# Performance work log

Measured on AMD Instinct MI355X. Metric: run time of the kernel, lower is better.

Reference implementation:

```python
import jax, jax.numpy as jnp
import numpy as np

EPS = 1e-5
INF = 1e5


def setup_inputs() -> dict:
    key = jax.random.key(0)
    ks = iter(jax.random.split(key, 32))
    B, N, F, H, NH, C = 2, 384, 64, 64, 4, 32
    def lin(k, fi, fo):
        return jax.random.normal(k, (fi, fo), jnp.float32) / np.sqrt(fi).astype(np.float32)
    d = {}
    d['h'] = jax.random.normal(next(ks), (B, N, F), jnp.float32)
    d['x'] = jax.random.normal(next(ks), (B, N, 3), jnp.float32)
    # edge_model (ConcatenationFilter): Linear(2F+1,H), SiLU, Linear(H,H), SiLU
    d['We0'] = lin(next(ks), 2 * F + 1, H); d['be0'] = jnp.zeros(H, jnp.float32)
    d['We1'] = lin(next(ks), H, H);         d['be1'] = jnp.zeros(H, jnp.float32)
    # semantic_attention_mlp: Linear(H, n_heads), LeakyReLU(0.2)
    d['Ws'] = lin(next(ks), H, NH);         d['bs'] = jnp.zeros(NH, jnp.float32)
    # coefficients_mlp: Linear(H,H), SiLU, Linear(H,C)
    d['Wc0'] = lin(next(ks), H, H);         d['bc0'] = jnp.zeros(H, jnp.float32)
    d['Wc1'] = lin(next(ks), H, C);         d['bc1'] = jnp.zeros(C, jnp.float32)
    # post_norm_mlp: Linear(C,H), SiLU, Linear(H,H)
    d['Wp0'] = lin(next(ks), C, H);         d['bp0'] = jnp.zeros(H, jnp.float32)
    d['Wp1'] = lin(next(ks), H, H);         d['bp1'] = jnp.zeros(H, jnp.float32)
    # coordinate_mlp: Linear(H,H), SiLU, Linear(H,1,bias=False) init gain 1e-3
    d['Wx0'] = lin(next(ks), H, H);         d['bx0'] = jnp.zeros(H, jnp.float32)
    d['Wx1'] = lin(next(ks), H, 1) * 1e-3
    # node_mlp: Linear(NH*H + H + F, H), SiLU, Linear(H, F)
    d['Wn0'] = lin(next(ks), NH * H + H + F, H); d['bn0'] = jnp.zeros(H, jnp.float32)
    d['Wn1'] = lin(next(ks), H, F);         d['bn1'] = jnp.zeros(F, jnp.float32)
    d['log_gamma'] = jnp.zeros(NH, jnp.float32)
    return d


def _forward(h, x, We0, be0, We1, be1, Ws, bs, Wc0, bc0, Wc1, bc1,
             Wp0, bp0, Wp1, bp1, Wx0, bx0, Wx1, Wn0, bn0, Wn1, bn1, log_gamma):
    B, N, F = h.shape
    silu = jax.nn.silu

    # pairwise displacements and distances: (B,N,N,3), (B,N,N,1)
    x_minus_xt = x[:, :, None, :] - x[:, None, :, :]
    norm = jnp.sqrt(jnp.sum(x_minus_xt * x_minus_xt, axis=-1, keepdims=True) + EPS)

    # pairwise node-feature concat + distance -> edge MLP (ConcatenationFilter)
    hi = jnp.broadcast_to(h[:, :, None, :], (B, N, N, F))
    hj = jnp.broadcast_to(h[:, None, :, :], (B, N, N, F))
    e_in = jnp.concatenate([hi, hj, norm], axis=-1)           # (B,N,N,2F+1)
    h_e = silu(silu(e_in @ We0 + be0) @ We1 + be1)            # (B,N,N,H)

    eye = jnp.eye(N, dtype=h.dtype)[None, :, :, None]         # mask self-edges

    # euclidean attention per head, softmax over neighbors j (axis=-2)
    eu = jax.nn.softmax(-(norm + INF * eye) * jnp.exp(log_gamma), axis=-2)  # (B,N,N,NH)
    # semantic attention
    sem_logits = jax.nn.leaky_relu(h_e @ Ws + bs, 0.2) - INF * eye
    sem = jax.nn.softmax(sem_logits, axis=-2)                 # (B,N,N,NH)
    comb = eu * sem
    comb = comb / (jnp.sum(comb, axis=-2, keepdims=True) + EPS)

    # attention-weighted multi-head edge features, aggregated over neighbors
    h_e_att = (comb[..., :, None] * h_e[..., None, :]).reshape(B, N, N, -1)  # (B,N,N,NH*H)
    h_e_agg = jnp.sum(h_e_att, axis=-2)                       # (B,N,NH*H)

    # spatial attention: equivariant combinations of unit direction vectors
    coeff = silu(h_e @ Wc0 + bc0) @ Wc1 + bc1                 # (B,N,N,C)
    x_hat = x_minus_xt / (norm + EPS)                         # (B,N,N,3)
    combinations = coeff[..., :, None] * x_hat[..., None, :]  # (B,N,N,C,3)
    comb_sum = jnp.mean(combinations, axis=2)                 # mean over j -> (B,N,C,3)
    comb_norm = jnp.sum(comb_sum * comb_sum, axis=-1)         # (B,N,C)
    h_comb = silu(comb_norm @ Wp0 + bp0) @ Wp1 + bp1          # (B,N,H)

    # node update (residual)
    node_in = jnp.concatenate([h, h_e_agg, h_comb], axis=-1)
    h_out = h + (silu(node_in @ Wn0 + bn0) @ Wn1 + bn1)

    # coordinate update: scalar-gated displacements, mean over neighbors
    scale = silu(h_e @ Wx0 + bx0) @ Wx1                       # (B,N,N,1)
    x_out = x + jnp.mean(x_minus_xt * scale, axis=2)          # (B,N,3)
    return h_out, x_out


def reference(h, x, We0, be0, We1, be1, Ws, bs, Wc0, bc0, Wc1, bc1,
              Wp0, bp0, Wp1, bp1, Wx0, bx0, Wx1, Wn0, bn0, Wn1, bn1, log_gamma):
    return _forward(h, x, We0, be0, We1, be1, Ws, bs, Wc0, bc0, Wc1, bc1,
                    Wp0, bp0, Wp1, bp1, Wx0, bx0, Wx1, Wn0, bn0, Wn1, bn1, log_gamma)
```

## Files before the change

### kernel.cpp

```cpp
#include <hip/hip_runtime.h>

#define NPT 384
#define NB 2
#define NROW (NB*NPT)
#define NT 6
#define HOFF 49152
#define RECB 1024
#define REC_OFF 424960

typedef unsigned short u16;
typedef unsigned int u32;
typedef __bf16 bf16x8 __attribute__((ext_vector_type(8)));
typedef float f32x4 __attribute__((ext_vector_type(4)));

struct alignas(16) U4 { u32 x, y, z, w; };

constexpr float kEPS = 1e-5f;
constexpr float kINF = 1e5f;

__device__ __forceinline__ u16 f2b(float f) { __bf16 b = (__bf16)f; return __builtin_bit_cast(u16, b); }
__device__ __forceinline__ u32 pk2(float lo, float hi) { return (u32)f2b(lo) | ((u32)f2b(hi) << 16); }
__device__ __forceinline__ float b2f(u32 u) { return __uint_as_float(u << 16); }
__device__ __forceinline__ float silu_f(float v) { return v * __builtin_amdgcn_rcpf(1.f + __expf(-v)); }
__device__ __forceinline__ float wredmax(float v) {
#pragma unroll
  for (int m = 32; m >= 1; m >>= 1) v = fmaxf(v, __shfl_xor(v, m, 64));
  return v;
}
__device__ __forceinline__ float wredsum(float v) {
#pragma unroll
  for (int m = 32; m >= 1; m >>= 1) v += __shfl_xor(v, m, 64);
  return v;
}
__device__ __forceinline__ void up8(U4 u, float* f) {
  f[0] = b2f(u.x & 0xffffu); f[1] = b2f(u.x >> 16);
  f[2] = b2f(u.y & 0xffffu); f[3] = b2f(u.y >> 16);
  f[4] = b2f(u.z & 0xffffu); f[5] = b2f(u.z >> 16);
  f[6] = b2f(u.w & 0xffffu); f[7] = b2f(u.w >> 16);
}

__global__ __launch_bounds__(64) void sake_prep(
    const float* __restrict__ h, const float* __restrict__ We0,
    const float* __restrict__ be0, const float* __restrict__ We1,
    const float* __restrict__ Wc0, const float* __restrict__ Wc1,
    const float* __restrict__ Wx0, const float* __restrict__ Ws,
    float* __restrict__ U, float* __restrict__ V, u16* __restrict__ WT)
{
  const int t = threadIdx.x;
  const int blk = blockIdx.x;
  if (blk < NROW) {
    __shared__ float hs[64];
    hs[t] = h[blk * 64 + t];
    __syncthreads();
    float u = be0[t], v = 0.f;
#pragma unroll 8
    for (int k = 0; k < 64; k++) {
      float hv = hs[k];
      u = fmaf(hv, We0[k * 64 + t], u);
      v = fmaf(hv, We0[(64 + k) * 64 + t], v);
    }
    U[blk * 64 + t] = u;
    V[blk * 64 + t] = v;
  } else {
    const int wsel = blk - NROW;
    if (wsel == 4) {
      u16* dst = WT + 14336;
      for (int o = t; o < 16 * 64; o += 64) {
        int c = o >> 6, k = o & 63;
        dst[o] = (c < 4) ? f2b(Ws[k * 4 + c]) : (u16)0;
      }
      return;
    }
    const float* src; int nout; u16* dst;
    if      (wsel == 0) { src = We1; nout = 64; dst = WT;         }
    else if (wsel == 1) { src = Wc0; nout = 64; dst = WT + 4096;  }
    else if (wsel == 2) { src = Wx0; nout = 64; dst = WT + 8192;  }
    else                { src = Wc1; nout = 32; dst = WT + 12288; }
    const int total = 64 * nout;
    for (int o = t; o < total; o += 64) {
      int n = o >> 6, k = o & 63;
      dst[o] = f2b(src[k * nout + n]);
    }
  }
}

struct MainArgs {
  const float *x, *U, *V;
  const u16 *We1T, *Wc0T, *Wx0T, *Wc1T, *WsPT;
  const float *We0, *bs, *be1, *bc0, *bc1, *bx0, *Wx1, *log_gamma;
  char* rec;
};

__device__ __forceinline__ void readB(const u16* tile, int j, int kg, bf16x8& f0, bf16x8& f1) {
  const int r7 = j & 7;
  f0 = *(const bf16x8*)(tile + j * 64 + ((kg ^ r7) << 3));
  f1 = *(const bf16x8*)(tile + j * 64 + (((kg + 4) ^ r7) << 3));
}

template<int NNT, bool SILU_, int NCH, bool DUALT>
__device__ __forceinline__ void gemmT8(const u16* __restrict__ wG, const float* __restrict__ biasG,
                                       bf16x8 bf0, bf16x8 bf1, u16* out, u16* oTT,
                                       int j, int kg, int l15, int nbase)
{
  const int jm = j & (NCH - 1);
#pragma unroll
  for (int nt = 0; nt < NNT; nt++) {
    const int nrow = nbase + (nt << 4) + l15;
    bf16x8 a0 = *(const bf16x8*)(wG + nrow * 64 + (kg << 3));
    bf16x8 a1 = *(const bf16x8*)(wG + nrow * 64 + 32 + (kg << 3));
    f32x4 acc = {0.f, 0.f, 0.f, 0.f};
    acc = __builtin_amdgcn_mfma_f32_16x16x32_bf16(a0, bf0, acc, 0, 0, 0);
    acc = __builtin_amdgcn_mfma_f32_16x16x32_bf16(a1, bf1, acc, 0, 0, 0);
    const int n0 = nbase + (nt << 4) + (kg << 2);
    const float4 bv = *(const float4*)(biasG + n0);
    float s0, s1, s2, s3;
    if constexpr (SILU_) {
      s0 = silu_f(acc[0] + bv.x); s1 = silu_f(acc[1] + bv.y);
      s2 = silu_f(acc[2] + bv.z); s3 = silu_f(acc[3] + bv.w);
    } else {
      s0 = acc[0] + bv.x; s1 = acc[1] + bv.y;
      s2 = acc[2] + bv.z; s3 = acc[3] + bv.w;
    }
    const u16 q0 = f2b(s0), q1 = f2b(s1), q2 = f2b(s2), q3 = f2b(s3);
    u32 pkx = (u32)q0 | ((u32)q1 << 16), pky = (u32)q2 | ((u32)q3 << 16);
    const int c = n0 >> 3;
    u32* dst = (u32*)(out + j * (NCH * 8) + (((c ^ jm) << 3) + (n0 & 7)));
    dst[0] = pkx; dst[1] = pky;
    if constexpr (DUALT) {
      const int jq = (j >> 3), j7 = j & 7;
      const u16 qs[4] = {q0, q1, q2, q3};
#pragma unroll
      for (int r = 0; r < 4; r++) {
        const int f = n0 + r;
        oTT[f * 64 + ((jq ^ (f & 7)) << 3) + j7] = qs[r];
      }
    }
  }
}

__global__ __launch_bounds__(512, 8) void sake_main(MainArgs A)
{
  __shared__ __align__(16) u16 buf0[64 * 64];
  __shared__ __align__(16) u16 hes[64 * 64];
  __shared__ __align__(16) u16 hesT[64 * 64];
  __shared__ __align__(16) u16 coeff[64 * 32];
  __shared__ __align__(16) u16 E_lds[16 * 64];
  __shared__ float raw_lds[64 * 5];
  __shared__ float disp[64][3];
  __shared__ float nrm_s[64];

  const int t = threadIdx.x;
  const int w = t >> 6, lane = t & 63;
  const int rs = w >> 1, ch = w & 1;
  const int kg = lane >> 4, l15 = lane & 15;
  const int bt = blockIdx.x;
  const int i = bt % NPT;
  const int bj = bt / NPT;
  const int jt = bj % NT, b = bj / NT;
  const int bi = b * NPT + i;
  const int j0 = jt << 6;
  char* rec = A.rec + (size_t)(bi * NT + jt) * RECB;

  const int jj3 = t >> 3, q8 = t & 7;
  {
    const int jrow = j0 + jj3;
    const float* xp = &A.x[(b * NPT + jrow) * 3];
    const float xj0 = xp[0], xj1 = xp[1], xj2 = xp[2];
    const float xi0 = A.x[bi * 3 + 0], xi1 = A.x[bi * 3 + 1], xi2 = A.x[bi * 3 + 2];
    const float4* vp = (const float4*)(A.V + (size_t)(b * NPT + jrow) * 64 + q8 * 8);
    const float4 v0_ = vp[0], v1_ = vp[1];
    const float4* Up = (const float4*)(A.U + bi * 64 + q8 * 8);
    const float4 u0_ = Up[0], u1_ = Up[1];
    const float4* Wd = (const float4*)(A.We0 + 128 * 64 + q8 * 8);
    const float4 w0_ = Wd[0], w1_ = Wd[1];
    float dx0 = xi0 - xj0, dx1 = xi1 - xj1, dx2 = xi2 - xj2;
    float nr = sqrtf(fmaf(dx0, dx0, fmaf(dx1, dx1, fmaf(dx2, dx2, kEPS))));
    if (q8 == 0) { disp[jj3][0] = dx0; disp[jj3][1] = dx1; disp[jj3][2] = dx2; nrm_s[jj3] = nr; }
    float vv[8] = {v0_.x, v0_.y, v0_.z, v0_.w, v1_.x, v1_.y, v1_.z, v1_.w};
    float uu[8] = {u0_.x, u0_.y, u0_.z, u0_.w, u1_.x, u1_.y, u1_.z, u1_.w};
    float ww[8] = {w0_.x, w0_.y, w0_.z, w0_.w, w1_.x, w1_.y, w1_.z, w1_.w};
    float sv[8];
#pragma unroll
    for (int e = 0; e < 8; e++) sv[e] = silu_f(uu[e] + vv[e] + nr * ww[e]);
    U4 u4;
    u4.x = pk2(sv[0], sv[1]); u4.y = pk2(sv[2], sv[3]);
    u4.z = pk2(sv[4], sv[5]); u4.w = pk2(sv[6], sv[7]);
    *(U4*)(buf0 + jj3 * 64 + ((q8 ^ (jj3 & 7)) << 3)) = u4;
  }
  __syncthreads();

  const int jrow16 = (rs << 4) + l15;
  const int nb64 = ch << 5;

  {
    bf16x8 bh0, bh1;
    readB(buf0, jrow16, kg, bh0, bh1);
    gemmT8<2, true, 8, true>(A.We1T, A.be1, bh0, bh1, hes, hesT, jrow16, kg, l15, nb64);
  }
  __syncthreads();

  bf16x8 he0, he1;
  readB(hes, jrow16, kg, he0, he1);

  gemmT8<2, true, 8, false>(A.Wc0T, A.bc0, he0, he1, buf0, nullptr, jrow16, kg, l15, nb64);
  __syncthreads();

  {
    bf16x8 c10, c11;
    readB(buf0, jrow16, kg, c10, c11);
    gemmT8<1, false, 4, false>(A.Wc1T, A.bc1, c10, c11, coeff, nullptr, jrow16, kg, l15, ch << 4);
  }
  if (ch == 0) {
    const int m0 = rs << 4;
    const int arow = m0 + l15;
    const int r7a = arow & 7;
    bf16x8 a0 = *(const bf16x8*)(hes + arow * 64 + ((kg ^ r7a) << 3));
    bf16x8 a1 = *(const bf16x8*)(hes + arow * 64 + (((kg + 4) ^ r7a) << 3));
    const u16* wrow = A.WsPT + l15 * 64;
    bf16x8 b0 = *(const bf16x8*)(wrow + (kg << 3));
    bf16x8 b1 = *(const bf16x8*)(wrow + 32 + (kg << 3));
    f32x4 acc = {0.f, 0.f, 0.f, 0.f};
    acc = __builtin_amdgcn_mfma_f32_16x16x32_bf16(a0, b0, acc, 0, 0, 0);
    acc = __builtin_amdgcn_mfma_f32_16x16x32_bf16(a1, b1, acc, 0, 0, 0);
    if (l15 < 4) {
#pragma unroll
      for (int r = 0; r < 4; r++)
        raw_lds[(m0 + (kg << 2) + r) * 5 + l15] = acc[r];
    }
  }
  __syncthreads();

  float cA0 = 0, cA1 = 0, cA2 = 0, xA0 = 0, xA1 = 0, xA2 = 0;
  {
    const int c = t & 31, g = t >> 5;
    const int cc = c >> 3, ce = c & 7;
#pragma unroll
    for (int it = 0; it < 4; ++it) {
      const int jj = (g << 2) + it;
      const float s = b2f(coeff[jj * 32 + ((cc ^ (jj & 3)) << 3) + ce]) *
                      __builtin_amdgcn_rcpf(nrm_s[jj] + kEPS);
      cA0 = fmaf(s, disp[jj][0], cA0);
      cA1 = fmaf(s, disp[jj][1], cA1);
      cA2 = fmaf(s, disp[jj][2], cA2);
    }
  }
  gemmT8<2, true, 8, false>(A.Wx0T, A.bx0, he0, he1, buf0, nullptr, jrow16, kg, l15, nb64);
  __syncthreads();

  float mL_r = 0.f, SL_r = 0.f, mb_r = 0.f, Sb_r = 0.f, Sa_r = 0.f;
  if (w < 4) {
    const int jj = lane, head = w;
    float raw = raw_lds[jj * 5 + head] + A.bs[head];
    float bsem = (raw > 0.f) ? raw : 0.2f * raw;
    const bool self = (j0 + jj) == i;
    if (self) bsem -= kINF;
    const float gam = __expf(A.log_gamma[head]);
    const float aeu = -(nrm_s[jj] + (self ? kINF : 0.f)) * gam;
    const float L = aeu + bsem;
    const float mL = wredmax(L);
    const float eL = __expf(L - mL);
    const float SL = wredsum(eL);
    const float mb = wredmax(bsem);
    const float Sb = wredsum(__expf(bsem - mb));
    const float Sa = wredsum(__expf(aeu));
    E_lds[head * 64 + (((jj >> 3) ^ head) << 3) + (jj & 7)] = f2b(eL);
    mL_r = mL; SL_r = SL; mb_r = mb; Sb_r = Sb; Sa_r = Sa;
  } else {
    const int tp = t - 256;
    const int jj = tp >> 2, q4 = tp & 3;
    const int r7 = jj & 7;
    float acc = 0.f;
#pragma unroll
    for (int c2 = 0; c2 < 2; c2++) {
      const int c = q4 * 2 + c2;
      U4 u = *(const U4*)(buf0 + jj * 64 + ((c ^ r7) << 3));
      float f8[8]; up8(u, f8);
      const float4* wx = (const float4*)(A.Wx1 + c * 8);
      const float4 wxa = wx[0], wxb = wx[1];
      acc = fmaf(f8[0], wxa.x, acc); acc = fmaf(f8[1], wxa.y, acc);
      acc = fmaf(f8[2], wxa.z, acc); acc = fmaf(f8[3], wxa.w, acc);
      acc = fmaf(f8[4], wxb.x, acc); acc = fmaf(f8[5], wxb.y, acc);
      acc = fmaf(f8[6], wxb.z, acc); acc = fmaf(f8[7], wxb.w, acc);
    }
    acc += __shfl_xor(acc, 1, 64);
    acc += __shfl_xor(acc, 2, 64);
    if (q4 == 0) {
      xA0 = disp[jj][0] * acc;
      xA1 = disp[jj][1] * acc;
      xA2 = disp[jj][2] * acc;
    }
  }
  if (w < 4 && lane == 0) {
    float* sp = (float*)(rec + 908) + w * 5;
    sp[0] = mL_r; sp[1] = SL_r; sp[2] = mb_r; sp[3] = Sb_r; sp[4] = Sa_r;
  }
  __syncthreads();

  float* cascr = (float*)buf0;
  float* xscr = (float*)hes;
  cascr[t * 3 + 0] = cA0; cascr[t * 3 + 1] = cA1; cascr[t * 3 + 2] = cA2;
  if (w >= 4 && ((t - 256) & 3) == 0) {
    const int jj = (t - 256) >> 2;
    xscr[jj * 3 + 0] = xA0; xscr[jj * 3 + 1] = xA1; xscr[jj * 3 + 2] = xA2;
  }
  if (w < 4) {
    const int erow = l15;
    const int e7 = erow & 7;
    bf16x8 ea0 = *(const bf16x8*)(E_lds + erow * 64 + ((kg ^ e7) << 3));
    bf16x8 ea1 = *(const bf16x8*)(E_lds + erow * 64 + (((kg + 4) ^ e7) << 3));
    const int f = (w << 4) + l15;
    const int f7 = f & 7;
    bf16x8 hb0 = *(const bf16x8*)(hesT + f * 64 + ((kg ^ f7) << 3));
    bf16x8 hb1 = *(const bf16x8*)(hesT + f * 64 + (((kg + 4) ^ f7) << 3));
    f32x4 aF = {0.f, 0.f, 0.f, 0.f};
    aF = __builtin_amdgcn_mfma_f32_16x16x32_bf16(ea0, hb0, aF, 0, 0, 0);
    aF = __builtin_amdgcn_mfma_f32_16x16x32_bf16(ea1, hb1, aF, 0, 0, 0);
    if (kg == 0) {
      u16* rA = (u16*)rec;
#pragma unroll
      for (int r = 0; r < 4; r++) rA[r * 64 + f] = f2b(aF[r]);
    }
  }
  __syncthreads();

  if (t < 96) {
    const int c = t & 31, d = t >> 5;
    float s = 0.f;
#pragma unroll
    for (int g = 0; g < 16; g++) s += cascr[(g * 32 + c) * 3 + d];
    ((float*)(rec + 512))[d * 32 + c] = s;
  } else if (t < 99) {
    const int d = t - 96;
    float s = 0.f;
    for (int k = 0; k < 64; k++) s += xscr[k * 3 + d];
    ((float*)(rec + 896))[d] = s;
  }
}

struct MergeArgs {
  const float *h, *x, *Wp0, *bp0, *Wp1, *bp1, *Wn0, *bn0, *Wn1, *bn1;
  const char* rec;
  float* out;
};

__global__ __launch_bounds__(256) void sake_merge(MergeArgs M)
{
  __shared__ float sc[NT][20];
  __shared__ float wAl[NT][4];
  __shared__ float coefh[4];
  __shared__ float node_in[384];
  __shared__ float cmv[96];
  __shared__ float nrm32[32];
  __shared__ float t0s[64];
  __shared__ float scr[256];

  const int t = threadIdx.x;
  const int bi = blockIdx.x;
  const char* rb = M.rec + (size_t)bi * NT * RECB;

  if (t < NT * 20) {
    const int tt = t / 20, k = t % 20;
    sc[tt][k] = ((const float*)(rb + tt * RECB + 908))[k];
  }
  if (t < 64) node_in[t] = M.h[bi * 64 + t];
  __syncthreads();
  if (t < 4) {
    const int hh = t;
    float mL = -1e30f, mb = -1e30f;
    for (int tt = 0; tt < NT; tt++) {
      mL = fmaxf(mL, sc[tt][hh * 5 + 0]);
      mb = fmaxf(mb, sc[tt][hh * 5 + 2]);
    }
    float SL = 0.f, Sb = 0.f, Sa = 0.f;
    for (int tt = 0; tt < NT; tt++) {
      const float wa = __expf(sc[tt][hh * 5 + 0] - mL);
      wAl[tt][hh] = wa;
      SL = fmaf(wa, sc[tt][hh * 5 + 1], SL);
      Sb = fmaf(__expf(sc[tt][hh * 5 + 2] - mb), sc[tt][hh * 5 + 3], Sb);
      Sa += sc[tt][hh * 5 + 4];
    }
    const float Ff = __expf(mL - mb);
    coefh[hh] = Ff / fmaf(SL, Ff, kEPS * Sa * Sb);
  }
  __syncthreads();
  {
    const int hh = t >> 6, f = t & 63;
    float s = 0.f;
#pragma unroll
    for (int tt = 0; tt < NT; tt++)
      s = fmaf(wAl[tt][hh], b2f(((const u16*)(rb + tt * RECB))[hh * 64 + f]), s);
    node_in[64 + hh * 64 + f] = s * coefh[hh];
  }
  if (t < 96) {
    float s = 0.f;
#pragma unroll
    for (int tt = 0; tt < NT; tt++) s += ((const float*)(rb + tt * RECB + 512))[t];
    cmv[t] = s * (1.f / 384.f);
  }
  if (t >= 128 && t < 131) {
    const int d = t - 128;
    float s = 0.f;
#pragma unroll
    for (int tt = 0; tt < NT; tt++) s += ((const float*)(rb + tt * RECB + 896))[d];
    M.out[HOFF + bi * 3 + d] = M.x[bi * 3 + d] + s * (1.f / 384.f);
  }
  __syncthreads();
  if (t < 32) {
    const float v0 = cmv[t], v1 = cmv[32 + t], v2 = cmv[64 + t];
    nrm32[t] = v0 * v0 + v1 * v1 + v2 * v2;
  }
  __syncthreads();
  if (t < 64) {
    float a = M.bp0[t];
    for (int c = 0; c < 32; c++) a = fmaf(nrm32[c], M.Wp0[c * 64 + t], a);
    t0s[t] = silu_f(a);
  }
  __syncthreads();
  if (t < 64) {
    float a = M.bp1[t];
    for (int k = 0; k < 64; k++) a = fmaf(t0s[k], M.Wp1[k * 64 + t], a);
    node_in[320 + t] = a;
  }
  __syncthreads();
  {
    const int f = t & 63, q = t >> 6;
    float a = 0.f;
    const int k0 = q * 96;
    for (int k = 0; k < 96; k++) a = fmaf(node_in[k0 + k], M.Wn0[(k0 + k) * 64 + f], a);
    scr[t] = a;
  }
  __syncthreads();
  if (t < 64) {
    const float s = scr[t] + scr[64 + t] + scr[128 + t] + scr[192 + t] + M.bn0[t];
    t0s[t] = silu_f(s);
  }
  __syncthreads();
  if (t < 64) {
    float a = M.bn1[t];
    for (int k = 0; k < 64; k++) a = fmaf(t0s[k], M.Wn1[k * 64 + t], a);
    M.out[bi * 64 + t] = M.h[bi * 64 + t] + a;
  }
}

extern "C" void kernel_launch(void* const* d_in, const int* in_sizes, int n_in,
                              void* d_out, int out_size, void* d_ws, size_t ws_size,
                              hipStream_t stream)
{
  (void)in_sizes; (void)n_in; (void)out_size; (void)ws_size;
  const float* h   = (const float*)d_in[0];
  const float* x   = (const float*)d_in[1];
  const float* We0 = (const float*)d_in[2];
  const float* be0 = (const float*)d_in[3];
  const float* We1 = (const float*)d_in[4];
  const float* be1 = (const float*)d_in[5];
  const float* Ws  = (const float*)d_in[6];
  const float* bs  = (const float*)d_in[7];
  const float* Wc0 = (const float*)d_in[8];
  const float* bc0 = (const float*)d_in[9];
  const float* Wc1 = (const float*)d_in[10];
  const float* bc1 = (const float*)d_in[11];
  const float* Wp0 = (const float*)d_in[12];
  const float* bp0 = (const float*)d_in[13];
  const float* Wp1 = (const float*)d_in[14];
  const float* bp1 = (const float*)d_in[15];
  const float* Wx0 = (const float*)d_in[16];
  const float* bx0 = (const float*)d_in[17];
  const float* Wx1 = (const float*)d_in[18];
  const float* Wn0 = (const float*)d_in[19];
  const float* bn0 = (const float*)d_in[20];
  const float* Wn1 = (const float*)d_in[21];
  const float* bn1 = (const float*)d_in[22];
  const float* lg  = (const float*)d_in[23];

  float* U = (float*)d_ws;
  float* V = U + NROW * 64;
  u16* WT = (u16*)(V + NROW * 64);
  char* rec = (char*)d_ws + REC_OFF;

  sake_prep<<<NROW + 5, 64, 0, stream>>>(h, We0, be0, We1, Wc0, Wc1, Wx0, Ws, U, V, WT);

  MainArgs A;
  A.x = x; A.U = U; A.V = V;
  A.We1T = WT; A.Wc0T = WT + 4096; A.Wx0T = WT + 8192; A.Wc1T = WT + 12288;
  A.WsPT = WT + 14336;
  A.We0 = We0; A.bs = bs; A.be1 = be1; A.bc0 = bc0; A.bc1 = bc1;
  A.bx0 = bx0; A.Wx1 = Wx1; A.log_gamma = lg;
  A.rec = rec;
  sake_main<<<NROW * NT, 512, 0, stream>>>(A);

  MergeArgs Mg;
  Mg.h = h; Mg.x = x;
  Mg.Wp0 = Wp0; Mg.bp0 = bp0; Mg.Wp1 = Wp1; Mg.bp1 = bp1;
  Mg.Wn0 = Wn0; Mg.bn0 = bn0; Mg.Wn1 = Wn1; Mg.bn1 = bn1;
  Mg.rec = rec; Mg.out = (float*)d_out;
  sake_merge<<<NROW, 256, 0, stream>>>(Mg);
}
```

Before: 99.94 us.

## Split waves between coefficient and coordinate MLPs, fuse Wx1, drop softmax max reductions

Waves 0-3 now run the Wc0/Wc1 GEMMs while waves 4-7 run the Wx0 GEMM concurrently. The waves 4-7 path fuses SiLU and the Wx1 dot product in registers, which removes a separate GEMM stage, its LDS round trip and one barrier. The per-head softmax statistics no longer subtract a wave maximum: the stored maxima are written as zero and only three sums are reduced. This saves shuffle reductions but risks overflow if logits are large. The inverse norm is precomputed once per row, and the coefficient-vector accumulation moves to waves 4-7 with wider per-thread loops.

```diff
diff --git a/kernel.cpp b/kernel.cpp
--- a/kernel.cpp
+++ b/kernel.cpp
@@ -22,22 +22,6 @@
 __device__ __forceinline__ u32 pk2(float lo, float hi) { return (u32)f2b(lo) | ((u32)f2b(hi) << 16); }
 __device__ __forceinline__ float b2f(u32 u) { return __uint_as_float(u << 16); }
 __device__ __forceinline__ float silu_f(float v) { return v * __builtin_amdgcn_rcpf(1.f + __expf(-v)); }
-__device__ __forceinline__ float wredmax(float v) {
-#pragma unroll
-  for (int m = 32; m >= 1; m >>= 1) v = fmaxf(v, __shfl_xor(v, m, 64));
-  return v;
-}
-__device__ __forceinline__ float wredsum(float v) {
-#pragma unroll
-  for (int m = 32; m >= 1; m >>= 1) v += __shfl_xor(v, m, 64);
-  return v;
-}
-__device__ __forceinline__ void up8(U4 u, float* f) {
-  f[0] = b2f(u.x & 0xffffu); f[1] = b2f(u.x >> 16);
-  f[2] = b2f(u.y & 0xffffu); f[3] = b2f(u.y >> 16);
-  f[4] = b2f(u.z & 0xffffu); f[5] = b2f(u.z >> 16);
-  f[6] = b2f(u.w & 0xffffu); f[7] = b2f(u.w >> 16);
-}
 
 __global__ __launch_bounds__(64) void sake_prep(
     const float* __restrict__ h, const float* __restrict__ We0,
@@ -147,11 +131,10 @@
   __shared__ __align__(16) u16 E_lds[16 * 64];
   __shared__ float raw_lds[64 * 5];
   __shared__ float disp[64][3];
-  __shared__ float nrm_s[64];
+  __shared__ float nrm_s[64], invn_s[64];
 
   const int t = threadIdx.x;
   const int w = t >> 6, lane = t & 63;
-  const int rs = w >> 1, ch = w & 1;
   const int kg = lane >> 4, l15 = lane & 15;
   const int bt = blockIdx.x;
   const int i = bt % NPT;
@@ -175,7 +158,10 @@
     const float4 w0_ = Wd[0], w1_ = Wd[1];
     float dx0 = xi0 - xj0, dx1 = xi1 - xj1, dx2 = xi2 - xj2;
     float nr = sqrtf(fmaf(dx0, dx0, fmaf(dx1, dx1, fmaf(dx2, dx2, kEPS))));
-    if (q8 == 0) { disp[jj3][0] = dx0; disp[jj3][1] = dx1; disp[jj3][2] = dx2; nrm_s[jj3] = nr; }
+    if (q8 == 0) {
+      disp[jj3][0] = dx0; disp[jj3][1] = dx1; disp[jj3][2] = dx2;
+      nrm_s[jj3] = nr; invn_s[jj3] = __builtin_amdgcn_rcpf(nr + kEPS);
+    }
     float vv[8] = {v0_.x, v0_.y, v0_.z, v0_.w, v1_.x, v1_.y, v1_.z, v1_.w};
     float uu[8] = {u0_.x, u0_.y, u0_.z, u0_.w, u1_.x, u1_.y, u1_.z, u1_.w};
     float ww[8] = {w0_.x, w0_.y, w0_.z, w0_.w, w1_.x, w1_.y, w1_.z, w1_.w};
@@ -189,29 +175,59 @@
   }
   __syncthreads();
 
-  const int jrow16 = (rs << 4) + l15;
-  const int nb64 = ch << 5;
-
   {
+    const int rs = w >> 1, ch = w & 1;
+    const int jr = (rs << 4) + l15;
     bf16x8 bh0, bh1;
-    readB(buf0, jrow16, kg, bh0, bh1);
-    gemmT8<2, true, 8, true>(A.We1T, A.be1, bh0, bh1, hes, hesT, jrow16, kg, l15, nb64);
-  }
-  __syncthreads();
-
-  bf16x8 he0, he1;
-  readB(hes, jrow16, kg, he0, he1);
-
-  gemmT8<2, true, 8, false>(A.Wc0T, A.bc0, he0, he1, buf0, nullptr, jrow16, kg, l15, nb64);
-  __syncthreads();
-
+    readB(buf0, jr, kg, bh0, bh1);
+    gemmT8<2, true, 8, true>(A.We1T, A.be1, bh0, bh1, hes, hesT, jr, kg, l15, ch << 5);
+  }
+  __syncthreads();
+
+  const int stripe = w & 3;
+  const int jrow16 = (stripe << 4) + l15;
+
+  float xA0 = 0, xA1 = 0, xA2 = 0;
   {
+    bf16x8 he0, he1;
+    readB(hes, jrow16, kg, he0, he1);
+    if (w < 4) {
+      gemmT8<4, true, 8, false>(A.Wc0T, A.bc0, he0, he1, buf0, nullptr, jrow16, kg, l15, 0);
+    } else {
+      float sacc = 0.f;
+#pragma unroll
+      for (int nt = 0; nt < 4; nt++) {
+        const int nrow = (nt << 4) + l15;
+        bf16x8 a0 = *(const bf16x8*)(A.Wx0T + nrow * 64 + (kg << 3));
+        bf16x8 a1 = *(const bf16x8*)(A.Wx0T + nrow * 64 + 32 + (kg << 3));
+        f32x4 acc = {0.f, 0.f, 0.f, 0.f};
+        acc = __builtin_amdgcn_mfma_f32_16x16x32_bf16(a0, he0, acc, 0, 0, 0);
+        acc = __builtin_amdgcn_mfma_f32_16x16x32_bf16(a1, he1, acc, 0, 0, 0);
+        const int n0 = (nt << 4) + (kg << 2);
+        const float4 bv = *(const float4*)(A.bx0 + n0);
+        const float4 wx = *(const float4*)(A.Wx1 + n0);
+        sacc = fmaf(silu_f(acc[0] + bv.x), wx.x, sacc);
+        sacc = fmaf(silu_f(acc[1] + bv.y), wx.y, sacc);
+        sacc = fmaf(silu_f(acc[2] + bv.z), wx.z, sacc);
+        sacc = fmaf(silu_f(acc[3] + bv.w), wx.w, sacc);
+      }
+      sacc += __shfl_xor(sacc, 16, 64);
+      sacc += __shfl_xor(sacc, 32, 64);
+      if (kg == 0) {
+        xA0 = disp[jrow16][0] * sacc;
+        xA1 = disp[jrow16][1] * sacc;
+        xA2 = disp[jrow16][2] * sacc;
+      }
+    }
+  }
+  __syncthreads();
+
+  if (w < 4) {
     bf16x8 c10, c11;
     readB(buf0, jrow16, kg, c10, c11);
-    gemmT8<1, false, 4, false>(A.Wc1T, A.bc1, c10, c11, coeff, nullptr, jrow16, kg, l15, ch << 4);
-  }
-  if (ch == 0) {
-    const int m0 = rs << 4;
+    gemmT8<2, false, 4, false>(A.Wc1T, A.bc1, c10, c11, coeff, nullptr, jrow16, kg, l15, 0);
+  } else {
+    const int m0 = stripe << 4;
     const int arow = m0 + l15;
     const int r7a = arow & 7;
     bf16x8 a0 = *(const bf16x8*)(hes + arow * 64 + ((kg ^ r7a) << 3));
@@ -230,24 +246,7 @@
   }
   __syncthreads();
 
-  float cA0 = 0, cA1 = 0, cA2 = 0, xA0 = 0, xA1 = 0, xA2 = 0;
-  {
-    const int c = t & 31, g = t >> 5;
-    const int cc = c >> 3, ce = c & 7;
-#pragma unroll
-    for (int it = 0; it < 4; ++it) {
-      const int jj = (g << 2) + it;
-      const float s = b2f(coeff[jj * 32 + ((cc ^ (jj & 3)) << 3) + ce]) *
-                      __builtin_amdgcn_rcpf(nrm_s[jj] + kEPS);
-      cA0 = fmaf(s, disp[jj][0], cA0);
-      cA1 = fmaf(s, disp[jj][1], cA1);
-      cA2 = fmaf(s, disp[jj][2], cA2);
-    }
-  }
-  gemmT8<2, true, 8, false>(A.Wx0T, A.bx0, he0, he1, buf0, nullptr, jrow16, kg, l15, nb64);
-  __syncthreads();
-
-  float mL_r = 0.f, SL_r = 0.f, mb_r = 0.f, Sb_r = 0.f, Sa_r = 0.f;
+  float cA0 = 0, cA1 = 0, cA2 = 0;
   if (w < 4) {
     const int jj = lane, head = w;
     float raw = raw_lds[jj * 5 + head] + A.bs[head];
@@ -256,53 +255,38 @@
     if (self) bsem -= kINF;
     const float gam = __expf(A.log_gamma[head]);
     const float aeu = -(nrm_s[jj] + (self ? kINF : 0.f)) * gam;
-    const float L = aeu + bsem;
-    const float mL = wredmax(L);
-    const float eL = __expf(L - mL);
-    const float SL = wredsum(eL);
-    const float mb = wredmax(bsem);
-    const float Sb = wredsum(__expf(bsem - mb));
-    const float Sa = wredsum(__expf(aeu));
+    const float eL = __expf(aeu + bsem);
+    const float eB = __expf(bsem);
+    const float eA = __expf(aeu);
+    float sL = eL, sB = eB, sA = eA;
+#pragma unroll
+    for (int m = 32; m >= 1; m >>= 1) {
+      sL += __shfl_xor(sL, m, 64);
+      sB += __shfl_xor(sB, m, 64);
+      sA += __shfl_xor(sA, m, 64);
+    }
     E_lds[head * 64 + (((jj >> 3) ^ head) << 3) + (jj & 7)] = f2b(eL);
-    mL_r = mL; SL_r = SL; mb_r = mb; Sb_r = Sb; Sa_r = Sa;
+    if (lane == 0) {
+      float* sp = (float*)(rec + 908) + head * 5;
+      sp[0] = 0.f; sp[1] = sL; sp[2] = 0.f; sp[3] = sB; sp[4] = sA;
+    }
   } else {
     const int tp = t - 256;
-    const int jj = tp >> 2, q4 = tp & 3;
-    const int r7 = jj & 7;
-    float acc = 0.f;
-#pragma unroll
-    for (int c2 = 0; c2 < 2; c2++) {
-      const int c = q4 * 2 + c2;
-      U4 u = *(const U4*)(buf0 + jj * 64 + ((c ^ r7) << 3));
-      float f8[8]; up8(u, f8);
-      const float4* wx = (const float4*)(A.Wx1 + c * 8);
-      const float4 wxa = wx[0], wxb = wx[1];
-      acc = fmaf(f8[0], wxa.x, acc); acc = fmaf(f8[1], wxa.y, acc);
-      acc = fmaf(f8[2], wxa.z, acc); acc = fmaf(f8[3], wxa.w, acc);
-      acc = fmaf(f8[4], wxb.x, acc); acc = fmaf(f8[5], wxb.y, acc);
-      acc = fmaf(f8[6], wxb.z, acc); acc = fmaf(f8[7], wxb.w, acc);
-    }
-    acc += __shfl_xor(acc, 1, 64);
-    acc += __shfl_xor(acc, 2, 64);
-    if (q4 == 0) {
-      xA0 = disp[jj][0] * acc;
-      xA1 = disp[jj][1] * acc;
-      xA2 = disp[jj][2] * acc;
-    }
-  }
-  if (w < 4 && lane == 0) {
-    float* sp = (float*)(rec + 908) + w * 5;
-    sp[0] = mL_r; sp[1] = SL_r; sp[2] = mb_r; sp[3] = Sb_r; sp[4] = Sa_r;
+    const int c = tp & 31, g = tp >> 5;
+    const int cc = c >> 3, ce = c & 7;
+#pragma unroll
+    for (int it = 0; it < 8; ++it) {
+      const int jj = (g << 3) + it;
+      const float s = b2f(coeff[jj * 32 + ((cc ^ (jj & 3)) << 3) + ce]) * invn_s[jj];
+      cA0 = fmaf(s, disp[jj][0], cA0);
+      cA1 = fmaf(s, disp[jj][1], cA1);
+      cA2 = fmaf(s, disp[jj][2], cA2);
+    }
   }
   __syncthreads();
 
   float* cascr = (float*)buf0;
-  float* xscr = (float*)hes;
-  cascr[t * 3 + 0] = cA0; cascr[t * 3 + 1] = cA1; cascr[t * 3 + 2] = cA2;
-  if (w >= 4 && ((t - 256) & 3) == 0) {
-    const int jj = (t - 256) >> 2;
-    xscr[jj * 3 + 0] = xA0; xscr[jj * 3 + 1] = xA1; xscr[jj * 3 + 2] = xA2;
-  }
+  float* xscr = (float*)raw_lds;
   if (w < 4) {
     const int erow = l15;
     const int e7 = erow & 7;
@@ -320,6 +304,12 @@
 #pragma unroll
       for (int r = 0; r < 4; r++) rA[r * 64 + f] = f2b(aF[r]);
     }
+  } else {
+    const int tp = t - 256;
+    cascr[tp * 3 + 0] = cA0; cascr[tp * 3 + 1] = cA1; cascr[tp * 3 + 2] = cA2;
+    if (kg == 0) {
+      xscr[jrow16 * 3 + 0] = xA0; xscr[jrow16 * 3 + 1] = xA1; xscr[jrow16 * 3 + 2] = xA2;
+    }
   }
   __syncthreads();
 
@@ -327,7 +317,7 @@
     const int c = t & 31, d = t >> 5;
     float s = 0.f;
 #pragma unroll
-    for (int g = 0; g < 16; g++) s += cascr[(g * 32 + c) * 3 + d];
+    for (int g = 0; g < 8; g++) s += cascr[(g * 32 + c) * 3 + d];
     ((float*)(rec + 512))[d * 32 + c] = s;
   } else if (t < 99) {
     const int d = t - 96;
```

Measured after the change: 100.7 us. About the same (+0.7%).
